# Kernel optimization log

Measured on AMD Instinct MI355X. Metric: run time of the kernel, lower is better.

## Reference

```python
import jax, jax.numpy as jnp
import numpy as np

NUM_NODES = 50000

def setup_inputs() -> dict:
    key = jax.random.key(0)
    k1, k2 = jax.random.split(key)
    x = jax.random.normal(k1, (NUM_NODES, 64), dtype=jnp.float32)
    edge_index = jax.random.randint(k2, (2, 800000), 0, NUM_NODES, dtype=jnp.int64)
    return {"x": x, "edge_index": edge_index}

def reference(x, edge_index):
    # gather source-node features along edges, scatter-mean into target nodes
    row, col = edge_index[0], edge_index[1]
    num_nodes = x.shape[0]
    gathered = x[row]  # [E, D]
    summed = jax.ops.segment_sum(gathered, col, num_segments=num_nodes)  # [N, D]
    count = jax.ops.segment_sum(jnp.ones_like(col, dtype=x.dtype), col, num_segments=num_nodes)  # [N]
    # mean with divide-by-zero guard (matches torch_geometric scatter reduce='mean')
    out = summed / jnp.maximum(count, 1.0)[:, None]
    return out
```

## Files before the change

### kernel.cpp

```cpp
#include <hip/hip_runtime.h>

#define N_NODES 50000
#define DIM 64
#define NPB 32
#define NB 1563
#define NCHUNK 256
#define CAPB 1024
#define CAP 1024

typedef unsigned short ushort_t;

__device__ __forceinline__ ushort_t f32_to_bf16(float f) {
    unsigned u = __float_as_uint(f);
    u += 0x7FFFu + ((u >> 16) & 1u);
    return (ushort_t)(u >> 16);
}

__device__ __forceinline__ void acc_pair(float& a0, float& a1, unsigned u) {
    a0 += __uint_as_float(u << 16);
    a1 += __uint_as_float(u & 0xFFFF0000u);
}

__global__ void convert_init_kernel(const float* __restrict__ xf,
                                    ushort_t* __restrict__ xh,
                                    int* __restrict__ cursor, int n4) {
    int gt = blockIdx.x * blockDim.x + threadIdx.x;
    if (gt <= NB) cursor[gt] = gt * CAPB;
    for (int i = gt; i < n4; i += gridDim.x * blockDim.x) {
        float4 v = *reinterpret_cast<const float4*>(xf + (size_t)i * 4);
        ushort4 hh;
        hh.x = f32_to_bf16(v.x);
        hh.y = f32_to_bf16(v.y);
        hh.z = f32_to_bf16(v.z);
        hh.w = f32_to_bf16(v.w);
        *reinterpret_cast<ushort4*>(xh + (size_t)i * 4) = hh;
    }
}

__global__ void binning_kernel(const int* __restrict__ row,
                               const int* __restrict__ col,
                               int* __restrict__ cursor,
                               unsigned* __restrict__ packed,
                               int E, int chunk) {
    __shared__ int h[NB];
    __shared__ int lcur[NB];
    int c = blockIdx.x;
    int tid = threadIdx.x;
    for (int b = tid; b < NB; b += blockDim.x) h[b] = 0;
    __syncthreads();
    int beg = c * chunk, end = min(beg + chunk, E);
    int nfull = (end - beg) >> 2;
    for (int g = tid; g < nfull; g += blockDim.x) {
        int4 c4 = *reinterpret_cast<const int4*>(col + beg + g * 4);
        atomicAdd(&h[c4.x >> 5], 1);
        atomicAdd(&h[c4.y >> 5], 1);
        atomicAdd(&h[c4.z >> 5], 1);
        atomicAdd(&h[c4.w >> 5], 1);
    }
    for (int e = beg + nfull * 4 + tid; e < end; e += blockDim.x)
        atomicAdd(&h[col[e] >> 5], 1);
    __syncthreads();
    for (int b = tid; b < NB; b += blockDim.x) {
        int v = h[b];
        lcur[b] = (v > 0) ? atomicAdd(&cursor[b], v) : 0;
    }
    __syncthreads();
    for (int g = tid; g < nfull; g += blockDim.x) {
        int e = beg + g * 4;
        int4 d4 = *reinterpret_cast<const int4*>(col + e);
        int4 s4 = *reinterpret_cast<const int4*>(row + e);
        int p0 = atomicAdd(&lcur[d4.x >> 5], 1);
        packed[p0] = (unsigned)s4.x | ((unsigned)(d4.x & 31) << 16);
        int p1 = atomicAdd(&lcur[d4.y >> 5], 1);
        packed[p1] = (unsigned)s4.y | ((unsigned)(d4.y & 31) << 16);
        int p2 = atomicAdd(&lcur[d4.z >> 5], 1);
        packed[p2] = (unsigned)s4.z | ((unsigned)(d4.z & 31) << 16);
        int p3 = atomicAdd(&lcur[d4.w >> 5], 1);
        packed[p3] = (unsigned)s4.w | ((unsigned)(d4.w & 31) << 16);
    }
    for (int e = beg + nfull * 4 + tid; e < end; e += blockDim.x) {
        int d = col[e];
        int p = atomicAdd(&lcur[d >> 5], 1);
        packed[p] = (unsigned)row[e] | ((unsigned)(d & 31) << 16);
    }
}

template <bool BF16>
__global__ __launch_bounds__(512)
void aggregate_bucket_kernel(const float* __restrict__ xf,
                             const ushort_t* __restrict__ xh,
                             const unsigned* __restrict__ packed,
                             const int* __restrict__ cursor,
                             float* __restrict__ out) {
    __shared__ unsigned buf[CAP];
    __shared__ unsigned short srcs[CAP];
    __shared__ int hist[NPB];
    __shared__ int segoff[NPB];
    __shared__ int lcur[NPB];
    __shared__ int cnt_tot[NPB];

    int b = blockIdx.x;
    int tid = threadIdx.x;
    int lane = tid & 63;
    int wv = tid >> 6;
    int g8 = lane >> 3;
    int o = lane & 7;
    int seg_beg = b * CAPB;
    int seg_end = cursor[b];
    int node_base = b * NPB;
    int nnodes = min(NPB, N_NODES - node_base);

    float acc[4][8];
    #pragma unroll
    for (int r = 0; r < 4; ++r)
        #pragma unroll
        for (int k = 0; k < 8; ++k) acc[r][k] = 0.0f;
    if (tid < NPB) cnt_tot[tid] = 0;

    for (int cs = seg_beg; cs < seg_end; cs += CAP) {
        int m = min(CAP, seg_end - cs);
        __syncthreads();
        if (tid < NPB) hist[tid] = 0;
        __syncthreads();
        for (int i = tid; i < m; i += 512) {
            unsigned v = packed[cs + i];
            buf[i] = v;
            atomicAdd(&hist[v >> 16], 1);
        }
        __syncthreads();
        if (tid < NPB) {
            int v = hist[tid];
            int incl = v;
            #pragma unroll
            for (int ofs = 1; ofs < 32; ofs <<= 1) {
                int t = __shfl_up(incl, ofs);
                if (lane >= ofs) incl += t;
            }
            segoff[tid] = incl - v;
            lcur[tid] = incl - v;
            cnt_tot[tid] += v;
        }
        __syncthreads();
        for (int i = tid; i < m; i += 512) {
            unsigned v = buf[i];
            int p = atomicAdd(&lcur[v >> 16], 1);
            srcs[p] = (unsigned short)(v & 0xFFFF);
        }
        __syncthreads();
        #pragma unroll
        for (int r = 0; r < 4; ++r) {
            int ln = wv * 4 + r;
            int st = segoff[ln];
            int len = hist[ln];
            int j = 0;
            for (; j + 16 <= len; j += 16) {
                int s0 = srcs[st + j + g8];
                int s1 = srcs[st + j + 8 + g8];
                if (BF16) {
                    uint4 a0 = *reinterpret_cast<const uint4*>(xh + (size_t)s0 * DIM + o * 8);
                    uint4 a1 = *reinterpret_cast<const uint4*>(xh + (size_t)s1 * DIM + o * 8);
                    acc_pair(acc[r][0], acc[r][1], a0.x);
                    acc_pair(acc[r][2], acc[r][3], a0.y);
                    acc_pair(acc[r][4], acc[r][5], a0.z);
                    acc_pair(acc[r][6], acc[r][7], a0.w);
                    acc_pair(acc[r][0], acc[r][1], a1.x);
                    acc_pair(acc[r][2], acc[r][3], a1.y);
                    acc_pair(acc[r][4], acc[r][5], a1.z);
                    acc_pair(acc[r][6], acc[r][7], a1.w);
                } else {
                    float4 u0 = *reinterpret_cast<const float4*>(xf + (size_t)s0 * DIM + o * 8);
                    float4 u1 = *reinterpret_cast<const float4*>(xf + (size_t)s0 * DIM + o * 8 + 4);
                    float4 u2 = *reinterpret_cast<const float4*>(xf + (size_t)s1 * DIM + o * 8);
                    float4 u3 = *reinterpret_cast<const float4*>(xf + (size_t)s1 * DIM + o * 8 + 4);
                    acc[r][0] += u0.x + u2.x; acc[r][1] += u0.y + u2.y;
                    acc[r][2] += u0.z + u2.z; acc[r][3] += u0.w + u2.w;
                    acc[r][4] += u1.x + u3.x; acc[r][5] += u1.y + u3.y;
                    acc[r][6] += u1.z + u3.z; acc[r][7] += u1.w + u3.w;
                }
            }
            for (; j < len; j += 8) {
                if (j + g8 < len) {
                    int s = srcs[st + j + g8];
                    if (BF16) {
                        uint4 a0 = *reinterpret_cast<const uint4*>(xh + (size_t)s * DIM + o * 8);
                        acc_pair(acc[r][0], acc[r][1], a0.x);
                        acc_pair(acc[r][2], acc[r][3], a0.y);
                        acc_pair(acc[r][4], acc[r][5], a0.z);
                        acc_pair(acc[r][6], acc[r][7], a0.w);
                    } else {
                        float4 u0 = *reinterpret_cast<const float4*>(xf + (size_t)s * DIM + o * 8);
                        float4 u1 = *reinterpret_cast<const float4*>(xf + (size_t)s * DIM + o * 8 + 4);
                        acc[r][0] += u0.x; acc[r][1] += u0.y;
                        acc[r][2] += u0.z; acc[r][3] += u0.w;
                        acc[r][4] += u1.x; acc[r][5] += u1.y;
                        acc[r][6] += u1.z; acc[r][7] += u1.w;
                    }
                }
            }
        }
    }
    __syncthreads();
    #pragma unroll
    for (int r = 0; r < 4; ++r) {
        int ln = wv * 4 + r;
        #pragma unroll
        for (int k = 0; k < 8; ++k) {
            acc[r][k] += __shfl_xor(acc[r][k], 8);
            acc[r][k] += __shfl_xor(acc[r][k], 16);
            acc[r][k] += __shfl_xor(acc[r][k], 32);
        }
        if (g8 == 0 && ln < nnodes) {
            int c = cnt_tot[ln];
            float inv = (c > 0) ? 1.0f / (float)c : 0.0f;
            float4 lo = make_float4(acc[r][0] * inv, acc[r][1] * inv,
                                    acc[r][2] * inv, acc[r][3] * inv);
            float4 hi = make_float4(acc[r][4] * inv, acc[r][5] * inv,
                                    acc[r][6] * inv, acc[r][7] * inv);
            float* op = out + (size_t)(node_base + ln) * DIM + o * 8;
            *reinterpret_cast<float4*>(op) = lo;
            *reinterpret_cast<float4*>(op + 4) = hi;
        }
    }
}

extern "C" void kernel_launch(void* const* d_in, const int* in_sizes, int n_in,
                              void* d_out, int out_size, void* d_ws, size_t ws_size,
                              hipStream_t stream) {
    const float* x = (const float*)d_in[0];
    const int* edge_index = (const int*)d_in[1];
    int E = in_sizes[1] / 2;
    const int* row = edge_index;
    const int* col = edge_index + E;
    float* out = (float*)d_out;

    int chunk = (((E + NCHUNK - 1) / NCHUNK) + 3) & ~3;
    int n4 = N_NODES * DIM / 4;

    int* cursor      = (int*)d_ws;
    unsigned* packed = (unsigned*)(cursor + 1568);
    ushort_t* xh     = (ushort_t*)(packed + (size_t)NB * CAPB);
    size_t need_bf16 = (size_t)((char*)(xh + (size_t)N_NODES * DIM) - (char*)d_ws);
    bool use_bf16 = (ws_size >= need_bf16);

    convert_init_kernel<<<256, 1024, 0, stream>>>(x, xh, cursor, use_bf16 ? n4 : 0);
    binning_kernel<<<NCHUNK, 1024, 0, stream>>>(row, col, cursor, packed, E, chunk);
    if (use_bf16)
        aggregate_bucket_kernel<true><<<NB, 512, 0, stream>>>(x, xh, packed, cursor, out);
    else
        aggregate_bucket_kernel<false><<<NB, 512, 0, stream>>>(x, xh, packed, cursor, out);
}
```

Baseline: 58.41 us.

## Fuse bf16 conversion into binning kernel and drop LDS staging buffer

```diff
diff --git a/kernel.cpp b/kernel.cpp
--- a/kernel.cpp
+++ b/kernel.cpp
@@ -21,12 +21,23 @@
     a1 += __uint_as_float(u & 0xFFFF0000u);
 }
 
-__global__ void convert_init_kernel(const float* __restrict__ xf,
-                                    ushort_t* __restrict__ xh,
-                                    int* __restrict__ cursor, int n4) {
-    int gt = blockIdx.x * blockDim.x + threadIdx.x;
-    if (gt <= NB) cursor[gt] = gt * CAPB;
-    for (int i = gt; i < n4; i += gridDim.x * blockDim.x) {
+__global__ void init_cursor_kernel(int* __restrict__ cursor) {
+    int t = blockIdx.x * blockDim.x + threadIdx.x;
+    if (t <= NB) cursor[t] = t * CAPB;
+}
+
+__global__ void binning_kernel(const float* __restrict__ xf,
+                               ushort_t* __restrict__ xh,
+                               const int* __restrict__ row,
+                               const int* __restrict__ col,
+                               int* __restrict__ cursor,
+                               unsigned* __restrict__ packed,
+                               int E, int chunk, int n4) {
+    __shared__ int h[NB];
+    __shared__ int lcur[NB];
+    int c = blockIdx.x;
+    int tid = threadIdx.x;
+    for (int i = c * blockDim.x + tid; i < n4; i += gridDim.x * blockDim.x) {
         float4 v = *reinterpret_cast<const float4*>(xf + (size_t)i * 4);
         ushort4 hh;
         hh.x = f32_to_bf16(v.x);
@@ -35,17 +46,6 @@
         hh.w = f32_to_bf16(v.w);
         *reinterpret_cast<ushort4*>(xh + (size_t)i * 4) = hh;
     }
-}
-
-__global__ void binning_kernel(const int* __restrict__ row,
-                               const int* __restrict__ col,
-                               int* __restrict__ cursor,
-                               unsigned* __restrict__ packed,
-                               int E, int chunk) {
-    __shared__ int h[NB];
-    __shared__ int lcur[NB];
-    int c = blockIdx.x;
-    int tid = threadIdx.x;
     for (int b = tid; b < NB; b += blockDim.x) h[b] = 0;
     __syncthreads();
     int beg = c * chunk, end = min(beg + chunk, E);
@@ -92,7 +92,6 @@
                              const unsigned* __restrict__ packed,
                              const int* __restrict__ cursor,
                              float* __restrict__ out) {
-    __shared__ unsigned buf[CAP];
     __shared__ unsigned short srcs[CAP];
     __shared__ int hist[NPB];
     __shared__ int segoff[NPB];
@@ -122,10 +121,18 @@
         __syncthreads();
         if (tid < NPB) hist[tid] = 0;
         __syncthreads();
-        for (int i = tid; i < m; i += 512) {
-            unsigned v = packed[cs + i];
-            buf[i] = v;
-            atomicAdd(&hist[v >> 16], 1);
+        {
+            int nf = m >> 2;
+            const uint4* p4 = reinterpret_cast<const uint4*>(packed + cs);
+            for (int i = tid; i < nf; i += 512) {
+                uint4 v = p4[i];
+                atomicAdd(&hist[v.x >> 16], 1);
+                atomicAdd(&hist[v.y >> 16], 1);
+                atomicAdd(&hist[v.z >> 16], 1);
+                atomicAdd(&hist[v.w >> 16], 1);
+            }
+            for (int i = nf * 4 + tid; i < m; i += 512)
+                atomicAdd(&hist[packed[cs + i] >> 16], 1);
         }
         __syncthreads();
         if (tid < NPB) {
@@ -142,7 +149,7 @@
         }
         __syncthreads();
         for (int i = tid; i < m; i += 512) {
-            unsigned v = buf[i];
+            unsigned v = packed[cs + i];
             int p = atomicAdd(&lcur[v >> 16], 1);
             srcs[p] = (unsigned short)(v & 0xFFFF);
         }
@@ -242,8 +249,9 @@
     size_t need_bf16 = (size_t)((char*)(xh + (size_t)N_NODES * DIM) - (char*)d_ws);
     bool use_bf16 = (ws_size >= need_bf16);
 
-    convert_init_kernel<<<256, 1024, 0, stream>>>(x, xh, cursor, use_bf16 ? n4 : 0);
-    binning_kernel<<<NCHUNK, 1024, 0, stream>>>(row, col, cursor, packed, E, chunk);
+    init_cursor_kernel<<<7, 256, 0, stream>>>(cursor);
+    binning_kernel<<<NCHUNK, 1024, 0, stream>>>(x, xh, row, col, cursor, packed,
+                                                E, chunk, use_bf16 ? n4 : 0);
     if (use_bf16)
         aggregate_bucket_kernel<true><<<NB, 512, 0, stream>>>(x, xh, packed, cursor, out);
     else
```

Result: faster. 56.95 us, median of 3 (-2.5%).
